# Optimization experiments

Measured on AMD Instinct MI355X. Metric: run time of the kernel, lower is better.

## Reference

```python
import jax, jax.numpy as jnp
import numpy as np

N = 40962          # icosphere level-6 vertex count
E = 245772         # N * k (k=6 knn, directed)
MUL_IN = 8         # '8x0e + 8x1o' -> dim 8 + 24 = 32
MUL_OUT = 16       # '16x0e + 16x1o' -> dim 16 + 48 = 64
H = 64             # radial MLP hidden
WNUM = 4 * MUL_IN * MUL_OUT  # 512 per-edge TP weights (4 CG paths)
SQ3 = np.float32(np.sqrt(3.0))


def setup_inputs() -> dict:
    key = jax.random.key(0)
    ks = jax.random.split(key, 8)
    x = jax.random.normal(ks[0], (N, MUL_IN + 3 * MUL_IN), dtype=jnp.float32)
    pos = jax.random.normal(ks[1], (N, 3), dtype=jnp.float32)
    src = jax.random.randint(ks[2], (E,), 0, N)
    dst = jax.random.randint(ks[3], (E,), 0, N)
    edge_index = jnp.stack([src, dst]).astype(jnp.int32)
    W1 = jax.random.normal(ks[4], (1, H), dtype=jnp.float32)
    W2 = jax.random.normal(ks[5], (H, WNUM), dtype=jnp.float32)
    Ws = jax.random.normal(ks[6], (MUL_OUT, MUL_OUT), dtype=jnp.float32)
    k7, k8 = jax.random.split(ks[7])
    Wns = jax.random.normal(k7, (MUL_OUT, MUL_OUT), dtype=jnp.float32)
    Wg = jax.random.normal(k8, (MUL_OUT, MUL_OUT), dtype=jnp.float32)
    return {"x": x, "pos": pos, "edge_index": edge_index,
            "W1": W1, "W2": W2, "Ws": Ws, "Wns": Wns, "Wg": Wg}


def reference(x, pos, edge_index, W1, W2, Ws, Wns, Wg):
    src, dst = edge_index[0], edge_index[1]
    xs = x[:, :MUL_IN]                                  # (N, 8)  scalars (0e)
    xv = x[:, MUL_IN:].reshape(-1, MUL_IN, 3)           # (N, 8, 3) vectors (1o)

    # --- edge geometry + spherical harmonics (component-normalized, lmax=1) ---
    edge_vec = pos[dst] - pos[src]                      # (E, 3)
    edge_len = jnp.maximum(jnp.linalg.norm(edge_vec, axis=-1, keepdims=True), 1e-8)
    edge_dir = edge_vec / edge_len                      # (E, 3)
    Y1 = SQ3 * edge_dir                                 # l=1 SH; l=0 SH == 1

    # --- radial MLP -> per-edge tensor-product weights (shared_weights=False) ---
    h = jax.nn.silu(edge_len @ W1)                      # (E, H), fan_in = 1
    w = (h @ W2) * (1.0 / np.sqrt(np.float32(H)))       # (E, 512)
    wA, wB, wC, wD = [wi.reshape(-1, MUL_IN, MUL_OUT)
                      for wi in jnp.split(w, 4, axis=1)]

    xs_e = xs[src]                                      # (E, 8)   gather
    xv_e = xv[src]                                      # (E, 8, 3) gather
    norm = np.float32(1.0 / np.sqrt(2.0 * MUL_IN))      # path normalization

    # --- tensor product: 4 CG paths ---
    # 0e x 0e -> 0e  (CG = 1)
    pathA = jnp.einsum('eu,euw->ew', xs_e, wA)
    # 1o x 1o -> 0e  (CG_ij = delta_ij / sqrt(3))
    dot = jnp.einsum('eui,ei->eu', xv_e, Y1) * (1.0 / SQ3)
    pathB = jnp.einsum('eu,euw->ew', dot, wB)
    m_s = (pathA + pathB) * norm                        # (E, 16)
    # 0e x 1o -> 1o  (CG = identity)
    pathC = jnp.einsum('eu,euw->ew', xs_e, wC)[:, :, None] * Y1[:, None, :]
    # 1o x 0e -> 1o  (CG = identity)
    pathD = jnp.einsum('eui,euw->ewi', xv_e, wD)
    m_v = (pathC + pathD) * norm                        # (E, 16, 3)

    m = jnp.concatenate([m_s, m_v.reshape(-1, 3 * MUL_OUT)], axis=1)  # (E, 64)

    # --- scatter-add to destination nodes (index_add) ---
    out = jnp.zeros((x.shape[0], m.shape[1]), dtype=x.dtype).at[dst].add(m)

    # --- gated equivariant nonlinearity (o3.Linear with fan-in norm) ---
    lin_norm = np.float32(1.0 / np.sqrt(np.float32(MUL_OUT)))
    os_ = out[:, :MUL_OUT]                              # (N, 16)
    ov_ = out[:, MUL_OUT:].reshape(-1, MUL_OUT, 3)      # (N, 16, 3)
    s = jax.nn.silu(os_ @ Ws * lin_norm)                # (N, 16)
    ns = jnp.einsum('nui,uw->nwi', ov_, Wns) * lin_norm # (N, 16, 3)
    g = jax.nn.sigmoid(os_ @ Wg * lin_norm)             # (N, 16)
    gated = (g[:, :, None] * ns).reshape(-1, 3 * MUL_OUT)
    return jnp.concatenate([s, gated], axis=1)          # (N, 64)
```

## Files before the change

### kernel.cpp

```cpp
#include <hip/hip_runtime.h>
#include <math.h>

typedef _Float16 half8 __attribute__((ext_vector_type(8)));
typedef float floatx4 __attribute__((ext_vector_type(4)));

#define SQ3 1.7320508075688772f

__global__ __launch_bounds__(256) void prep_w2(const float* __restrict__ W2,
                                               _Float16* __restrict__ bw) {
    int t = blockIdx.x * 256 + threadIdx.x;
    if (t >= 32768) return;
    int i    = t & 7;
    int l    = (t >> 3) & 63;
    int s    = (t >> 9) & 1;
    int tt   = (t >> 10) & 7;
    int path = t >> 13;
    int k   = s * 32 + (l >> 4) * 8 + i;
    int col = path * 128 + tt * 16 + (l & 15);
    float scale = 0.03125f * (path == 2 ? SQ3 : 1.0f);
    bw[t] = (_Float16)(W2[k * 512 + col] * scale);
}

struct Pref {
    float4 xa;
    float psx, psy, psz, pdx, pdy, pdz;
    int di;
};

__device__ __forceinline__ Pref issue_loads(int tile, int E,
        const int* __restrict__ ei, const float* __restrict__ x,
        const float* __restrict__ pos, int tid) {
    Pref p;
    int el = tid >> 3, q = tid & 7;
    int eg = tile * 64 + el;
    int ec = (eg < E) ? eg : (E - 1);
    int si = ei[ec];
    p.di = ei[E + ec];
    p.xa = *reinterpret_cast<const float4*>(x + (size_t)si * 32 + q * 4);
    const float* ps = pos + (size_t)si * 3;
    const float* pd = pos + (size_t)p.di * 3;
    p.psx = ps[0]; p.psy = ps[1]; p.psz = ps[2];
    p.pdx = pd[0]; p.pdy = pd[1]; p.pdz = pd[2];
    return p;
}

__global__ __launch_bounds__(512, 4) void edge_kernel(
    const float* __restrict__ x, const float* __restrict__ pos,
    const int* __restrict__ ei, const float* __restrict__ W1,
    const _Float16* __restrict__ bw, float* __restrict__ out,
    int E, int ntiles)
{
    __shared__ float sW1[64];
    __shared__ __align__(16) float4 s_geo[64];
    __shared__ int s_dst[2][64];
    __shared__ __align__(16) float s_xs[64][12];
    __shared__ __align__(16) float s_xvp[3][64][12];
    __shared__ __align__(16) _Float16 s_hA[4][2][64][8];
    __shared__ __align__(16) _Float16 s_part[4][64][66];

    const int tid  = threadIdx.x;
    const int wave = tid >> 6;
    const int path = wave >> 1;
    const int th   = wave & 1;
    const int lane = tid & 63;
    const int ub   = th * 4;

    if (tid < 64) sW1[tid] = W1[tid];

    half8 bfrag[4][2];
    {
        const half8* bsrc = (const half8*)bw;
        #pragma unroll
        for (int tt = 0; tt < 4; ++tt)
            #pragma unroll
            for (int s = 0; s < 2; ++s)
                bfrag[tt][s] = bsrc[(size_t)path * 1024 + ((ub + tt) * 2 + s) * 64 + lane];
    }

    int tile = blockIdx.x;
    if (tile >= ntiles) return;
    Pref p = issue_loads(tile, E, ei, x, pos, tid);
    __syncthreads();

    int buf = 0;
    for (; tile < ntiles; tile += gridDim.x) {
        {
            int el = tid >> 3, q = tid & 7;
            float ex = p.pdx - p.psx;
            float ey = p.pdy - p.psy;
            float ez = p.pdz - p.psz;
            float len = fmaxf(sqrtf(ex * ex + ey * ey + ez * ez), 1e-8f);
            float inv = 1.0f / len;
            if (q == 0) {
                s_geo[el] = make_float4(ex * inv, ey * inv, ez * inv, len);
                s_dst[buf][el] = p.di;
            }
            if (q < 2) {
                *(float4*)&s_xs[el][q * 4] = p.xa;
            } else {
                float vals[4] = {p.xa.x, p.xa.y, p.xa.z, p.xa.w};
                #pragma unroll
                for (int j = 0; j < 4; ++j) {
                    int flat = (q - 2) * 4 + j;
                    int u  = (flat * 11) >> 5;
                    int ii = flat - 3 * u;
                    s_xvp[ii][el][u] = vals[j];
                }
            }
            int s  = q >> 2, kg = q & 3;
            int sub = el >> 4;
            int l   = kg * 16 + (el & 15);
            half8 ha;
            #pragma unroll
            for (int i = 0; i < 8; ++i) {
                float z = len * sW1[s * 32 + kg * 8 + i];
                ha[i] = (_Float16)(z / (1.0f + __expf(-z)));
            }
            *(half8*)&s_hA[sub][s][l][0] = ha;
        }
        __syncthreads();

        int nt = tile + gridDim.x;
        Pref pn;
        if (nt < ntiles) pn = issue_loads(nt, E, ei, x, pos, tid);

        const int wp  = lane & 15;
        const int er0 = (lane >> 4) * 4;
        #pragma unroll
        for (int sub = 0; sub < 4; ++sub) {
            half8 a0 = *(const half8*)&s_hA[sub][0][lane][0];
            half8 a1 = *(const half8*)&s_hA[sub][1][lane][0];
            floatx4 acc[4];
            #pragma unroll
            for (int tt = 0; tt < 4; ++tt) {
                floatx4 z = {0.f, 0.f, 0.f, 0.f};
                z = __builtin_amdgcn_mfma_f32_16x16x32_f16(a0, bfrag[tt][0], z, 0, 0, 0);
                acc[tt] = __builtin_amdgcn_mfma_f32_16x16x32_f16(a1, bfrag[tt][1], z, 0, 0, 0);
            }

            if (path == 0) {
                #pragma unroll
                for (int r = 0; r < 4; ++r) {
                    int e = sub * 16 + er0 + r;
                    float4 x0 = *(const float4*)&s_xs[e][ub];
                    float m = x0.x*acc[0][r] + x0.y*acc[1][r] + x0.z*acc[2][r] + x0.w*acc[3][r];
                    s_part[th][e][wp] = (_Float16)m;
                }
            } else if (path == 1) {
                #pragma unroll
                for (int r = 0; r < 4; ++r) {
                    int e = sub * 16 + er0 + r;
                    float4 g = s_geo[e];
                    float4 v0 = *(const float4*)&s_xvp[0][e][ub];
                    float4 v1 = *(const float4*)&s_xvp[1][e][ub];
                    float4 v2 = *(const float4*)&s_xvp[2][e][ub];
                    float d0 = v0.x*acc[0][r] + v0.y*acc[1][r] + v0.z*acc[2][r] + v0.w*acc[3][r];
                    float d1 = v1.x*acc[0][r] + v1.y*acc[1][r] + v1.z*acc[2][r] + v1.w*acc[3][r];
                    float d2 = v2.x*acc[0][r] + v2.y*acc[1][r] + v2.z*acc[2][r] + v2.w*acc[3][r];
                    s_part[2 + th][e][wp] = (_Float16)(g.x*d0 + g.y*d1 + g.z*d2);
                }
            } else if (path == 2) {
                #pragma unroll
                for (int r = 0; r < 4; ++r) {
                    int e = sub * 16 + er0 + r;
                    float4 x0 = *(const float4*)&s_xs[e][ub];
                    float4 g = s_geo[e];
                    float cw = x0.x*acc[0][r] + x0.y*acc[1][r] + x0.z*acc[2][r] + x0.w*acc[3][r];
                    s_part[th][e][16 + wp * 3 + 0] = (_Float16)(cw * g.x);
                    s_part[th][e][16 + wp * 3 + 1] = (_Float16)(cw * g.y);
                    s_part[th][e][16 + wp * 3 + 2] = (_Float16)(cw * g.z);
                }
            } else {
                #pragma unroll
                for (int r = 0; r < 4; ++r) {
                    int e = sub * 16 + er0 + r;
                    #pragma unroll
                    for (int i = 0; i < 3; ++i) {
                        float4 v0 = *(const float4*)&s_xvp[i][e][ub];
                        float mi = v0.x*acc[0][r] + v0.y*acc[1][r] + v0.z*acc[2][r] + v0.w*acc[3][r];
                        s_part[2 + th][e][16 + wp * 3 + i] = (_Float16)mi;
                    }
                }
            }
        }
        __syncthreads();

        {
            int c = tid & 63;
            int g = tid >> 6;
            #pragma unroll
            for (int k = 0; k < 8; ++k) {
                int e  = g * 8 + k;
                int eg = tile * 64 + e;
                if (eg < E) {
                    float v = (float)s_part[0][e][c] + (float)s_part[1][e][c]
                            + (float)s_part[2][e][c] + (float)s_part[3][e][c];
                    atomicAdd(out + (size_t)s_dst[buf][e] * 64 + c, v);
                }
            }
        }
        p = pn;
        buf ^= 1;
    }
}

__global__ __launch_bounds__(256) void node_kernel(
    float* __restrict__ out, const float* __restrict__ Ws,
    const float* __restrict__ Wns, const float* __restrict__ Wg, int N)
{
    int n = blockIdx.x * 256 + threadIdx.x;
    if (n >= N) return;
    float* row = out + (size_t)n * 64;

    float os[16], ov[48];
    #pragma unroll
    for (int q = 0; q < 4; ++q) {
        float4 v = *reinterpret_cast<const float4*>(row + q * 4);
        os[q*4+0]=v.x; os[q*4+1]=v.y; os[q*4+2]=v.z; os[q*4+3]=v.w;
    }
    #pragma unroll
    for (int q = 0; q < 12; ++q) {
        float4 v = *reinterpret_cast<const float4*>(row + 16 + q * 4);
        ov[q*4+0]=v.x; ov[q*4+1]=v.y; ov[q*4+2]=v.z; ov[q*4+3]=v.w;
    }

    float sres[16], gres[16];
    #pragma unroll
    for (int w = 0; w < 16; ++w) {
        float a = 0.f, b = 0.f;
        #pragma unroll
        for (int u = 0; u < 16; ++u) {
            float o_u = os[u];
            a += o_u * Ws[u * 16 + w];
            b += o_u * Wg[u * 16 + w];
        }
        a *= 0.25f; b *= 0.25f;
        sres[w] = a / (1.0f + __expf(-a));
        gres[w] = 1.0f / (1.0f + __expf(-b));
    }

    float gated[48];
    #pragma unroll
    for (int w = 0; w < 16; ++w) {
        float n0 = 0.f, n1 = 0.f, n2 = 0.f;
        #pragma unroll
        for (int u = 0; u < 16; ++u) {
            float wn = Wns[u * 16 + w];
            n0 += ov[u*3+0] * wn;
            n1 += ov[u*3+1] * wn;
            n2 += ov[u*3+2] * wn;
        }
        float gw = gres[w] * 0.25f;
        gated[w*3+0] = n0 * gw;
        gated[w*3+1] = n1 * gw;
        gated[w*3+2] = n2 * gw;
    }

    #pragma unroll
    for (int q = 0; q < 4; ++q) {
        float4 v = make_float4(sres[q*4+0], sres[q*4+1], sres[q*4+2], sres[q*4+3]);
        *reinterpret_cast<float4*>(row + q * 4) = v;
    }
    #pragma unroll
    for (int q = 0; q < 12; ++q) {
        float4 v = make_float4(gated[q*4+0], gated[q*4+1], gated[q*4+2], gated[q*4+3]);
        *reinterpret_cast<float4*>(row + 16 + q * 4) = v;
    }
}

extern "C" void kernel_launch(void* const* d_in, const int* in_sizes, int n_in,
                              void* d_out, int out_size, void* d_ws, size_t ws_size,
                              hipStream_t stream) {
    const float* x   = (const float*)d_in[0];
    const float* pos = (const float*)d_in[1];
    const int*   ei  = (const int*)d_in[2];
    const float* W1  = (const float*)d_in[3];
    const float* W2  = (const float*)d_in[4];
    const float* Ws  = (const float*)d_in[5];
    const float* Wns = (const float*)d_in[6];
    const float* Wg  = (const float*)d_in[7];

    int N = in_sizes[0] / 32;
    int E = in_sizes[2] / 2;
    int ntiles = (E + 63) / 64;
    float* out = (float*)d_out;
    _Float16* bw = (_Float16*)d_ws;

    hipMemsetAsync(out, 0, (size_t)N * 64 * sizeof(float), stream);
    prep_w2<<<128, 256, 0, stream>>>(W2, bw);
    int nblk = ntiles < 512 ? ntiles : 512;
    edge_kernel<<<nblk, 512, 0, stream>>>(x, pos, ei, W1, bw, out, E, ntiles);
    node_kernel<<<(N + 255) / 256, 256, 0, stream>>>(out, Ws, Wns, Wg, N);
}
```

Baseline: 107.8 us.

## Accumulate scatter in fp16 buffer with packed half2 atomics

Moves the scatter-add target from the fp32 output to an fp16 accumulation buffer in workspace. Each thread now reduces 8 contiguous channels for one edge with vectorized half8 LDS reads and issues four packed half2 atomic adds instead of eight fp32 atomics. The node kernel reads the fp16 accumulator and writes fp32 output. This cuts atomic traffic and memset size, but summing about six fp16 messages per node loses precision and risks overflow or tolerance failures.

```diff
diff --git a/kernel.cpp b/kernel.cpp
--- a/kernel.cpp
+++ b/kernel.cpp
@@ -1,4 +1,5 @@
 #include <hip/hip_runtime.h>
+#include <hip/hip_fp16.h>
 #include <math.h>
 
 typedef _Float16 half8 __attribute__((ext_vector_type(8)));
@@ -47,7 +48,7 @@
 __global__ __launch_bounds__(512, 4) void edge_kernel(
     const float* __restrict__ x, const float* __restrict__ pos,
     const int* __restrict__ ei, const float* __restrict__ W1,
-    const _Float16* __restrict__ bw, float* __restrict__ out,
+    const _Float16* __restrict__ bw, _Float16* __restrict__ accum,
     int E, int ntiles)
 {
     __shared__ float sW1[64];
@@ -56,7 +57,7 @@
     __shared__ __align__(16) float s_xs[64][12];
     __shared__ __align__(16) float s_xvp[3][64][12];
     __shared__ __align__(16) _Float16 s_hA[4][2][64][8];
-    __shared__ __align__(16) _Float16 s_part[4][64][66];
+    __shared__ __align__(16) _Float16 s_part[4][64][72];
 
     const int tid  = threadIdx.x;
     const int wave = tid >> 6;
@@ -186,16 +187,27 @@
         __syncthreads();
 
         {
-            int c = tid & 63;
-            int g = tid >> 6;
-            #pragma unroll
-            for (int k = 0; k < 8; ++k) {
-                int e  = g * 8 + k;
-                int eg = tile * 64 + e;
-                if (eg < E) {
-                    float v = (float)s_part[0][e][c] + (float)s_part[1][e][c]
-                            + (float)s_part[2][e][c] + (float)s_part[3][e][c];
-                    atomicAdd(out + (size_t)s_dst[buf][e] * 64 + c, v);
+            int e  = tid >> 3;
+            int q  = tid & 7;
+            int eg = tile * 64 + e;
+            if (eg < E) {
+                float v[8];
+                #pragma unroll
+                for (int j = 0; j < 8; ++j) v[j] = 0.f;
+                #pragma unroll
+                for (int g = 0; g < 4; ++g) {
+                    half8 pv = *(const half8*)&s_part[g][e][q * 8];
+                    #pragma unroll
+                    for (int j = 0; j < 8; ++j) v[j] += (float)pv[j];
+                }
+                __half2* base = reinterpret_cast<__half2*>(accum)
+                              + (size_t)s_dst[buf][e] * 32 + q * 4;
+                #pragma unroll
+                for (int k = 0; k < 4; ++k) {
+                    __half2 hv;
+                    hv.x = __float2half(v[2 * k]);
+                    hv.y = __float2half(v[2 * k + 1]);
+                    unsafeAtomicAdd(base + k, hv);
                 }
             }
         }
@@ -205,23 +217,26 @@
 }
 
 __global__ __launch_bounds__(256) void node_kernel(
-    float* __restrict__ out, const float* __restrict__ Ws,
-    const float* __restrict__ Wns, const float* __restrict__ Wg, int N)
+    const _Float16* __restrict__ accum, float* __restrict__ out,
+    const float* __restrict__ Ws, const float* __restrict__ Wns,
+    const float* __restrict__ Wg, int N)
 {
     int n = blockIdx.x * 256 + threadIdx.x;
     if (n >= N) return;
-    float* row = out + (size_t)n * 64;
+    const _Float16* row = accum + (size_t)n * 64;
 
     float os[16], ov[48];
     #pragma unroll
-    for (int q = 0; q < 4; ++q) {
-        float4 v = *reinterpret_cast<const float4*>(row + q * 4);
-        os[q*4+0]=v.x; os[q*4+1]=v.y; os[q*4+2]=v.z; os[q*4+3]=v.w;
-    }
-    #pragma unroll
-    for (int q = 0; q < 12; ++q) {
-        float4 v = *reinterpret_cast<const float4*>(row + 16 + q * 4);
-        ov[q*4+0]=v.x; ov[q*4+1]=v.y; ov[q*4+2]=v.z; ov[q*4+3]=v.w;
+    for (int q = 0; q < 2; ++q) {
+        half8 v = *reinterpret_cast<const half8*>(&row[q * 8]);
+        #pragma unroll
+        for (int j = 0; j < 8; ++j) os[q * 8 + j] = (float)v[j];
+    }
+    #pragma unroll
+    for (int q = 0; q < 6; ++q) {
+        half8 v = *reinterpret_cast<const half8*>(&row[16 + q * 8]);
+        #pragma unroll
+        for (int j = 0; j < 8; ++j) ov[q * 8 + j] = (float)v[j];
     }
 
     float sres[16], gres[16];
@@ -256,15 +271,16 @@
         gated[w*3+2] = n2 * gw;
     }
 
+    float* orow = out + (size_t)n * 64;
     #pragma unroll
     for (int q = 0; q < 4; ++q) {
         float4 v = make_float4(sres[q*4+0], sres[q*4+1], sres[q*4+2], sres[q*4+3]);
-        *reinterpret_cast<float4*>(row + q * 4) = v;
+        *reinterpret_cast<float4*>(orow + q * 4) = v;
     }
     #pragma unroll
     for (int q = 0; q < 12; ++q) {
         float4 v = make_float4(gated[q*4+0], gated[q*4+1], gated[q*4+2], gated[q*4+3]);
-        *reinterpret_cast<float4*>(row + 16 + q * 4) = v;
+        *reinterpret_cast<float4*>(orow + 16 + q * 4) = v;
     }
 }
 
@@ -284,11 +300,14 @@
     int E = in_sizes[2] / 2;
     int ntiles = (E + 63) / 64;
     float* out = (float*)d_out;
-    _Float16* bw = (_Float16*)d_ws;
-
-    hipMemsetAsync(out, 0, (size_t)N * 64 * sizeof(float), stream);
+    char* ws = (char*)d_ws;
+
+    _Float16* bw    = (_Float16*)ws;
+    _Float16* accum = (_Float16*)(ws + 65536);
+
+    (void)hipMemsetAsync(accum, 0, (size_t)N * 64 * sizeof(_Float16), stream);
     prep_w2<<<128, 256, 0, stream>>>(W2, bw);
     int nblk = ntiles < 512 ? ntiles : 512;
-    edge_kernel<<<nblk, 512, 0, stream>>>(x, pos, ei, W1, bw, out, E, ntiles);
-    node_kernel<<<(N + 255) / 256, 256, 0, stream>>>(out, Ws, Wns, Wg, N);
-}
+    edge_kernel<<<nblk, 512, 0, stream>>>(x, pos, ei, W1, bw, accum, E, ntiles);
+    node_kernel<<<(N + 255) / 256, 256, 0, stream>>>(accum, out, Ws, Wns, Wg, N);
+}
```

Measured after the change: 149.2 us. +38.5%, slower.
